# Optimization experiments

Measured on AMD Instinct MI355X. Metric: run time of the kernel, lower is better.

Reference implementation:

```python
import jax, jax.numpy as jnp
import numpy as np

B, L, C, H = 2, 2048, 1024, 16
D = C // H
THETA = 50000.0


def rotate_half(x):
    x1, x2 = jnp.split(x, 2, axis=-1)
    return jnp.concatenate((-x2, x1), axis=-1)


def rope_freqs(n, dim):
    inv_freq = 1.0 / (THETA ** (jnp.arange(0, dim, 2, dtype=jnp.float32) / dim))
    freqs = jnp.arange(n, dtype=jnp.float32)[:, None] * inv_freq[None, :]  # [n, dim//2]
    return jnp.concatenate((freqs, freqs), axis=-1)  # [n, dim]


def setup_inputs() -> dict:
    key = jax.random.key(0)
    ks = jax.random.split(key, 8)
    q = jax.random.normal(ks[0], (B, L, C), dtype=jnp.float32)
    mask = jax.random.randint(ks[1], (B, L), 0, 2) > 0
    mask = mask.at[:, 0].set(True)  # avoid fully-masked rows
    s = 1.0 / np.sqrt(C)
    Wq = jax.random.normal(ks[2], (C, C), dtype=jnp.float32) * s
    Wk = jax.random.normal(ks[3], (C, C), dtype=jnp.float32) * s
    Wv = jax.random.normal(ks[4], (C, C), dtype=jnp.float32) * s
    Wo = jax.random.normal(ks[5], (C, C), dtype=jnp.float32) * s
    bo = jnp.zeros((C,), dtype=jnp.float32)
    return {"q": q, "mask": mask, "Wq": Wq, "Wk": Wk, "Wv": Wv, "Wo": Wo, "bo": bo}


def reference(q, mask, Wq, Wk, Wv, Wo, bo):
    x = q
    # QKV projections (torch Linear: y = x @ W.T)
    def proj(W):
        y = jnp.einsum('blc,oc->blo', x, W)
        return y.reshape(B, L, H, D).transpose(0, 2, 1, 3)  # [B,H,L,D]
    qh, kh, vh = proj(Wq), proj(Wk), proj(Wv)
    # RoPE (L == S)
    pos = rope_freqs(L, D)  # [L, D]
    cos, sin = jnp.cos(pos), jnp.sin(pos)
    qh = qh * cos + rotate_half(qh) * sin
    kh = kh * cos + rotate_half(kh) * sin
    # masked SDPA with additive bias (-inf where mask is False)
    scale = 1.0 / np.sqrt(D)
    bias = jnp.where(mask[:, None, None, :], 0.0, -jnp.inf)  # [B,1,1,S]
    scores = jnp.einsum('bhld,bhsd->bhls', qh, kh) * scale + bias
    attn = jax.nn.softmax(scores, axis=-1)
    out = jnp.einsum('bhls,bhsd->bhld', attn, vh)
    out = out.transpose(0, 2, 1, 3).reshape(B, L, C)
    return jnp.einsum('blc,oc->blo', out, Wo) + bo
```

## Files before the change

kernel.cpp:

```cpp
#include <hip/hip_runtime.h>
#include <hip/hip_bf16.h>

typedef __hip_bfloat16 bf16;
typedef short bf16x8 __attribute__((ext_vector_type(8)));
typedef short bf16x4 __attribute__((ext_vector_type(4)));
typedef float floatx4 __attribute__((ext_vector_type(4)));

#define Bb 2
#define Ll 2048
#define Cc 1024
#define Hh 16
#define Dd 64
#define INVFREQ_LN 0.3381180763f
#define QSCALE 0.125f
#define NCONV 4096

#define GLD16(gp, lp) __builtin_amdgcn_global_load_lds( \
    (const __attribute__((address_space(1))) void*)(gp), \
    (__attribute__((address_space(3))) void*)(lp), 16, 0, 0)

__device__ inline short f2bf(float f) {
    __hip_bfloat16 h = __float2bfloat16(f);
    return *reinterpret_cast<short*>(&h);
}
__device__ inline short f2bf_rn(float f) {
    return (short)((__float_as_uint(f) + 0x8000u) >> 16);
}

__global__ __launch_bounds__(256) void convert_scan(
    const float* __restrict__ x, const float* __restrict__ wq,
    const float* __restrict__ wk, const float* __restrict__ wv,
    const float* __restrict__ wo,
    bf16* __restrict__ xb, bf16* __restrict__ wqkv, bf16* __restrict__ wob,
    const int* __restrict__ mask, int* __restrict__ cidx, int* __restrict__ valid)
{
    if (blockIdx.x >= NCONV) {
        const int b   = blockIdx.x - NCONV;
        const int tid = threadIdx.x;
        const int base = b * Ll + tid * 8;
        int m[8]; int s = 0;
        #pragma unroll
        for (int i = 0; i < 8; i++) { m[i] = mask[base + i] ? 1 : 0; s += m[i]; }
        const int lane = tid & 63;
        int xx = s;
        #pragma unroll
        for (int off = 1; off < 64; off <<= 1) {
            int y = __shfl_up(xx, off);
            if (lane >= off) xx += y;
        }
        __shared__ int wtot[4];
        if (lane == 63) wtot[tid >> 6] = xx;
        __syncthreads();
        int wbase = 0;
        const int w = tid >> 6;
        #pragma unroll
        for (int i = 0; i < 4; i++) if (i < w) wbase += wtot[i];
        int run = wbase + (xx - s);
        #pragma unroll
        for (int i = 0; i < 8; i++) { cidx[base + i] = run; run += m[i]; }
        if (tid == 255) valid[b] = run;
        return;
    }

    const int XN = (Bb * Ll * Cc) / 8;
    const int WN = (Cc * Cc) / 8;
    int i = blockIdx.x * 256 + threadIdx.x;
    const float* src; bf16* dst;
    if (i < XN)               { src = x  + (size_t)i * 8;                 dst = xb   + (size_t)i * 8; }
    else if (i < XN + WN)     { int j = i - XN;        src = wq + (size_t)j * 8; dst = wqkv + (size_t)j * 8; }
    else if (i < XN + 2*WN)   { int j = i - XN - WN;   src = wk + (size_t)j * 8; dst = wqkv + (size_t)Cc*Cc     + (size_t)j * 8; }
    else if (i < XN + 3*WN)   { int j = i - XN - 2*WN; src = wv + (size_t)j * 8; dst = wqkv + (size_t)Cc*Cc*2   + (size_t)j * 8; }
    else                      { int j = i - XN - 3*WN; src = wo + (size_t)j * 8; dst = wob  + (size_t)j * 8; }
    float4 a = *reinterpret_cast<const float4*>(src);
    float4 b = *reinterpret_cast<const float4*>(src + 4);
    float vv[8] = {a.x, a.y, a.z, a.w, b.x, b.y, b.z, b.w};
    bf16x8 o;
    #pragma unroll
    for (int t = 0; t < 8; t++) o[t] = f2bf(vv[t]);
    *reinterpret_cast<bf16x8*>(dst) = o;
}

template <int ROWS, int NTHREADS>
__device__ __forceinline__ void stage_swz(const bf16* __restrict__ g, int ldk,
                                          short* lds, int tid)
{
    #pragma unroll
    for (int s = 0; s < (ROWS * 4) / NTHREADS; s++) {
        const int idx = s * NTHREADS + tid;
        const int r   = idx >> 2;
        const int col = ((idx & 3) ^ ((r >> 1) & 3)) << 3;
        GLD16(g + (size_t)r * ldk + col, lds + idx * 8);
    }
}

#define SYNC_KEEP(N) do { \
    asm volatile("s_waitcnt vmcnt(" #N ")" ::: "memory"); \
    __builtin_amdgcn_s_barrier(); \
    asm volatile("" ::: "memory"); } while (0)

template <int MODE>
__global__ __launch_bounds__(256, 3) void gemm_mfma(
    const bf16* __restrict__ A, const bf16* __restrict__ W,
    bf16* __restrict__ qb, bf16* __restrict__ kb, bf16* __restrict__ vb,
    float* __restrict__ outf, const float* __restrict__ bias,
    const int* __restrict__ cmask, const int* __restrict__ cidx,
    int M, int N, int K)
{
    __shared__ __align__(16) short As[3][128 * 32];
    __shared__ __align__(16) short Bs[3][128 * 32];

    const int tid  = threadIdx.x;
    const int wave = tid >> 6;
    const int lane = tid & 63;
    const int l15  = lane & 15;
    const int quad = lane >> 4;
    const int wm   = wave >> 1;
    const int wn   = wave & 1;

    const int nbx = gridDim.x;
    const int nwg = nbx * gridDim.y;
    const int lin = blockIdx.y * nbx + blockIdx.x;
    const int cpx = nwg >> 3;
    const int swz = (lin & 7) * cpx + (lin >> 3);
    const int m0  = (swz / nbx) * 128;
    const int n0  = (swz % nbx) * 128;

    const bf16* Ag = A + (size_t)m0 * K;
    const bf16* Wg = W + (size_t)n0 * K;

    const int gsw = (quad ^ ((l15 >> 1) & 3)) << 3;

    floatx4 acc[4][4];
    #pragma unroll
    for (int mt = 0; mt < 4; mt++)
        #pragma unroll
        for (int nt = 0; nt < 4; nt++)
            #pragma unroll
            for (int r = 0; r < 4; r++) acc[mt][nt][r] = 0.f;

    const int T = K >> 5;

    stage_swz<128, 256>(Ag,      K, &As[0][0], tid);
    stage_swz<128, 256>(Wg,      K, &Bs[0][0], tid);
    stage_swz<128, 256>(Ag + 32, K, &As[1][0], tid);
    stage_swz<128, 256>(Wg + 32, K, &Bs[1][0], tid);
    SYNC_KEEP(4);

    int cur = 0;
    for (int t = 0; t < T; t++) {
        const short* Ac = &As[0][0] + cur * (128 * 32);
        const short* Bc = &Bs[0][0] + cur * (128 * 32);

        if (t + 2 < T) {
            int nb = cur + 2; if (nb >= 3) nb -= 3;
            const int kk = (t + 2) << 5;
            stage_swz<128, 256>(Ag + kk, K, &As[0][0] + nb * (128 * 32), tid);
            stage_swz<128, 256>(Wg + kk, K, &Bs[0][0] + nb * (128 * 32), tid);
        }

        bf16x8 bfr[4];
        #pragma unroll
        for (int nt = 0; nt < 4; nt++)
            bfr[nt] = *(const bf16x8*)(Bc + (wn * 64 + nt * 16 + l15) * 32 + gsw);

        __builtin_amdgcn_s_setprio(1);
        #pragma unroll
        for (int mt = 0; mt < 4; mt++) {
            bf16x8 af = *(const bf16x8*)(Ac + (wm * 64 + mt * 16 + l15) * 32 + gsw);
            #pragma unroll
            for (int nt = 0; nt < 4; nt++)
                acc[mt][nt] = __builtin_amdgcn_mfma_f32_16x16x32_bf16(
                    af, bfr[nt], acc[mt][nt], 0, 0, 0);
        }
        __builtin_amdgcn_s_setprio(0);

        if (t + 2 < T) SYNC_KEEP(4);
        else           SYNC_KEEP(0);

        cur = (cur + 1 == 3) ? 0 : cur + 1;
    }

    if constexpr (MODE == 1) {
        #pragma unroll
        for (int mt = 0; mt < 4; mt++)
            #pragma unroll
            for (int r = 0; r < 4; r++) {
                int row = m0 + wm * 64 + mt * 16 + quad * 4 + r;
                #pragma unroll
                for (int nt = 0; nt < 4; nt++) {
                    int col = n0 + wn * 64 + nt * 16 + l15;
                    outf[(size_t)row * N + col] = acc[mt][nt][r] + bias[col];
                }
            }
    } else {
        const int colbase = n0 + wn * 64;
        const int which   = colbase >> 10;
        const int hh      = (colbase & (Cc - 1)) >> 6;
        if (which == 2) {
            #pragma unroll
            for (int mt = 0; mt < 4; mt++)
                #pragma unroll
                for (int r = 0; r < 4; r++) {
                    int row = m0 + wm * 64 + mt * 16 + quad * 4 + r;
                    int b = row >> 11, l = row & (Ll - 1);
                    if (cmask[b * Ll + l]) {
                        int c = cidx[b * Ll + l];
                        size_t head = (size_t)(b * Hh + hh) * Dd * Ll;
                        int lbase = (c & ~63) | (c & 7);
                        int lg    = (c >> 3) & 7;
                        #pragma unroll
                        for (int nt = 0; nt < 4; nt++) {
                            int d = nt * 16 + l15;
                            int pos = lbase | ((lg ^ (d & 7)) << 3);
                            vb[head + (size_t)d * Ll + pos] = __float2bfloat16(acc[mt][nt][r]);
                        }
                    }
                }
        } else {
            bf16* dst = which ? kb : qb;
            const float qs = which ? 1.0f : QSCALE;
            const float base0 = __expf(-(float)l15 * INVFREQ_LN);
            const float base1 = __expf(-(float)(l15 + 16) * INVFREQ_LN);
            #pragma unroll
            for (int mt = 0; mt < 4; mt++)
                #pragma unroll
                for (int r = 0; r < 4; r++) {
                    int row = m0 + wm * 64 + mt * 16 + quad * 4 + r;
                    int b = row >> 11, l = row & (Ll - 1);
                    int cm = 1, c = l;
                    if (which == 1) {
                        cm = cmask[b * Ll + l];
                        c  = cidx[b * Ll + l];
                    }
                    if (cm) {
                        size_t rb = ((size_t)(b * Hh + hh) * Ll + c) * Dd;
                        #pragma unroll
                        for (int nt2 = 0; nt2 < 2; nt2++) {
                            float fr = (float)l * (nt2 ? base1 : base0);
                            float sn, cs;
                            __sincosf(fr, &sn, &cs);
                            float x1 = acc[mt][nt2][r];
                            float x2 = acc[mt][nt2 + 2][r];
                            float o1 = (x1 * cs - x2 * sn) * qs;
                            float o2 = (x2 * cs + x1 * sn) * qs;
                            int d1 = nt2 * 16 + l15;
                            int d2 = d1 + 32;
                            if (which == 1) {
                                int sw = c & 7;
                                int a1 = ((((d1 >> 3) ^ sw)) << 3) | (d1 & 7);
                                int a2 = ((((d2 >> 3) ^ sw)) << 3) | (d2 & 7);
                                dst[rb + a1] = __float2bfloat16(o1);
                                dst[rb + a2] = __float2bfloat16(o2);
                            } else {
                                dst[rb + d1] = __float2bfloat16(o1);
                                dst[rb + d2] = __float2bfloat16(o2);
                            }
                        }
                    }
                }
        }
    }
}

#define LSTR 72

__global__ __launch_bounds__(512) void attn_mfma(
    const bf16* __restrict__ q, const bf16* __restrict__ k, const bf16* __restrict__ vt,
    const int* __restrict__ valid, bf16* __restrict__ ctx)
{
    __shared__ __align__(16) short Ks[2][64 * 64];
    __shared__ __align__(16) short Vs[2][64 * 64];
    __shared__ __align__(16) short Ps[8][16 * LSTR];

    const int tid  = threadIdx.x;
    const int wave = tid >> 6;
    const int lane = tid & 63;
    const int l15  = lane & 15;
    const int quad = lane >> 4;

    const int bh = blockIdx.x & 31;
    const int q0 = (blockIdx.x >> 5) << 7;
    const int b  = bh >> 4;
    const int h  = bh & (Hh - 1);

    const int nvalid = valid[b];
    const int ntiles = (nvalid + 63) >> 6;

    const short* qb  = (const short*)(q  + (size_t)bh * Ll * Dd);
    const short* kb  = (const short*)(k  + (size_t)bh * Ll * Dd);
    const short* vtb = (const short*)(vt + (size_t)bh * Dd * Ll);

    const int qrow = q0 + wave * 16 + l15;
    bf16x8 qa0 = *(const bf16x8*)(qb + (size_t)qrow * Dd + quad * 8);
    bf16x8 qa1 = *(const bf16x8*)(qb + (size_t)qrow * Dd + 32 + quad * 8);

    const int g0 = ((quad ^ (l15 & 7)) << 3);
    const int g1 = (((quad + 4) ^ (l15 & 7)) << 3);

    const short* vgp = vtb + (size_t)(tid >> 3) * Ll + ((tid & 7) << 3);
    short* ksl = &Ks[0][0] + tid * 8;
    short* vsl = &Vs[0][0] + tid * 8;
    const int lbuf = 64 * 64;

    floatx4 O[4];
    float l_r = 0.f;
    #pragma unroll
    for (int nt = 0; nt < 4; nt++)
        #pragma unroll
        for (int r = 0; r < 4; r++) O[nt][r] = 0.f;

    GLD16(kb + tid * 8, ksl);
    GLD16(vgp, vsl);

    for (int t = 0; t < ntiles; t++) {
        const int cur = t & 1;
        __syncthreads();
        if (t + 1 < ntiles) {
            const int s1 = (t + 1) << 6;
            GLD16(kb + (size_t)s1 * Dd + tid * 8, ksl + (cur ^ 1) * lbuf);
            GLD16(vgp + s1,                       vsl + (cur ^ 1) * lbuf);
        }

        const short* Kc = &Ks[cur][0];
        const short* Vc = &Vs[cur][0];
        floatx4 S[4];
        #pragma unroll
        for (int nt = 0; nt < 4; nt++) {
            const short* krow = Kc + (nt * 16 + l15) * 64;
            bf16x8 ka0 = *(const bf16x8*)(krow + g0);
            bf16x8 ka1 = *(const bf16x8*)(krow + g1);
            floatx4 acc; acc[0] = acc[1] = acc[2] = acc[3] = 0.f;
            acc = __builtin_amdgcn_mfma_f32_16x16x32_bf16(ka0, qa0, acc, 0, 0, 0);
            acc = __builtin_amdgcn_mfma_f32_16x16x32_bf16(ka1, qa1, acc, 0, 0, 0);
            S[nt] = acc;
        }

        if (t + 1 < ntiles) {
            #pragma unroll
            for (int nt = 0; nt < 4; nt++) {
                bf16x4 pw;
                #pragma unroll
                for (int r = 0; r < 4; r++) {
                    float p = __expf(S[nt][r]);
                    l_r += p;
                    pw[r] = f2bf_rn(p);
                }
                *(bf16x4*)&Ps[wave][l15 * LSTR + nt * 16 + quad * 4] = pw;
            }
        } else {
            const int kbase = (t << 6) + quad * 4;
            #pragma unroll
            for (int nt = 0; nt < 4; nt++) {
                bf16x4 pw;
                #pragma unroll
                for (int r = 0; r < 4; r++) {
                    float p = (kbase + nt * 16 + r < nvalid) ? __expf(S[nt][r]) : 0.f;
                    l_r += p;
                    pw[r] = f2bf_rn(p);
                }
                *(bf16x4*)&Ps[wave][l15 * LSTR + nt * 16 + quad * 4] = pw;
            }
        }

        bf16x8 pb0 = *(const bf16x8*)&Ps[wave][l15 * LSTR + quad * 8];
        bf16x8 pb1 = *(const bf16x8*)&Ps[wave][l15 * LSTR + 32 + quad * 8];
        #pragma unroll
        for (int nt = 0; nt < 4; nt++) {
            const short* vrow = Vc + (nt * 16 + l15) * 64;
            bf16x8 va0 = *(const bf16x8*)(vrow + g0);
            bf16x8 va1 = *(const bf16x8*)(vrow + g1);
            O[nt] = __builtin_amdgcn_mfma_f32_16x16x32_bf16(va0, pb0, O[nt], 0, 0, 0);
            O[nt] = __builtin_amdgcn_mfma_f32_16x16x32_bf16(va1, pb1, O[nt], 0, 0, 0);
        }
    }

    float l = l_r;
    l += __shfl_xor(l, 16);
    l += __shfl_xor(l, 32);
    const float inv = 1.0f / l;

    {
        int row = q0 + wave * 16 + l15;
        short* cp = (short*)ctx + ((size_t)(b * Ll + row)) * Cc + h * Dd;
        #pragma unroll
        for (int nt = 0; nt < 4; nt++) {
            bf16x4 ov;
            #pragma unroll
            for (int r = 0; r < 4; r++) ov[r] = f2bf_rn(O[nt][r] * inv);
            *(bf16x4*)&cp[nt * 16 + quad * 4] = ov;
        }
    }
}

extern "C" void kernel_launch(void* const* d_in, const int* in_sizes, int n_in,
                              void* d_out, int out_size, void* d_ws, size_t ws_size,
                              hipStream_t stream) {
    const float* x    = (const float*)d_in[0];
    const int*   mask = (const int*)d_in[1];
    const float* Wq   = (const float*)d_in[2];
    const float* Wk   = (const float*)d_in[3];
    const float* Wv   = (const float*)d_in[4];
    const float* Wo   = (const float*)d_in[5];
    const float* bo   = (const float*)d_in[6];
    float* out = (float*)d_out;

    const size_t per = (size_t)Bb * Hh * Ll * Dd;
    bf16* qbuf = (bf16*)d_ws;
    bf16* kbuf = qbuf + per;
    bf16* vbuf = kbuf + per;
    bf16* xb   = vbuf + per;
    bf16* wqkv = xb + per;
    bf16* wob  = wqkv + (size_t)3 * Cc * Cc;
    int*  cidx   = (int*)(wob + (size_t)Cc * Cc);
    int*  cvalid = cidx + Bb * Ll;
    bf16* ctx  = xb;

    const int M = Bb * Ll;

    convert_scan<<<NCONV + Bb, 256, 0, stream>>>(
        x, Wq, Wk, Wv, Wo, xb, wqkv, wob, mask, cidx, cvalid);

    dim3 gQKV(3 * Cc / 128, M / 128);
    gemm_mfma<0><<<gQKV, 256, 0, stream>>>(xb, wqkv, qbuf, kbuf, vbuf,
                                           nullptr, nullptr, mask, cidx, M, 3 * Cc, Cc);

    attn_mfma<<<Bb * Hh * (Ll / 128), 512, 0, stream>>>(qbuf, kbuf, vbuf, cvalid, ctx);

    dim3 gOut(Cc / 128, M / 128);
    gemm_mfma<1><<<gOut, 256, 0, stream>>>(ctx, wob, nullptr, nullptr, nullptr,
                                           out, bo, nullptr, nullptr, M, Cc, Cc);
}
```

Baseline: 178.2 us.

## Split GEMM into specialized QKV 256x256 tile and output 64x128 tile kernels

Replaces the templated 128x128 GEMM with two specialized kernels. The QKV projection now uses 512-thread blocks with 256x256 tiles and a ping-pong schedule, splitting each k-step into two MFMA halves separated by barriers and interleaved with staged loads. The output projection uses smaller 64x128 tiles so it launches more blocks and fills the GPU better. The changes aim to raise data reuse and MFMA utilization in the large GEMM and occupancy in the small one, at the cost of more LDS, more registers and extra barriers per iteration.

```diff
diff --git a/kernel.cpp b/kernel.cpp
--- a/kernel.cpp
+++ b/kernel.cpp
@@ -93,20 +93,175 @@
     }
 }
 
-#define SYNC_KEEP(N) do { \
-    asm volatile("s_waitcnt vmcnt(" #N ")" ::: "memory"); \
-    __builtin_amdgcn_s_barrier(); \
-    asm volatile("" ::: "memory"); } while (0)
-
-template <int MODE>
-__global__ __launch_bounds__(256, 3) void gemm_mfma(
+#define VMCNT(N) asm volatile("s_waitcnt vmcnt(" #N ")" ::: "memory")
+
+__global__ __launch_bounds__(512, 2) void gemm_qkv(
     const bf16* __restrict__ A, const bf16* __restrict__ W,
     bf16* __restrict__ qb, bf16* __restrict__ kb, bf16* __restrict__ vb,
-    float* __restrict__ outf, const float* __restrict__ bias,
-    const int* __restrict__ cmask, const int* __restrict__ cidx,
-    int M, int N, int K)
+    const int* __restrict__ cmask, const int* __restrict__ cidx)
 {
-    __shared__ __align__(16) short As[3][128 * 32];
+    constexpr int K = Cc;
+    constexpr int T = K / 32;
+
+    __shared__ __align__(16) short As[3][256 * 32];
+    __shared__ __align__(16) short Bs[3][256 * 32];
+
+    const int tid  = threadIdx.x;
+    const int wave = tid >> 6;
+    const int lane = tid & 63;
+    const int l15  = lane & 15;
+    const int quad = lane >> 4;
+    const int wm   = wave >> 2;
+    const int wn   = wave & 3;
+
+    const int lin = blockIdx.y * 12 + blockIdx.x;
+    const int swz = (lin & 7) * 24 + (lin >> 3);
+    const int m0  = (swz / 12) * 256;
+    const int n0  = (swz % 12) * 256;
+
+    const bf16* Ag = A + (size_t)m0 * K;
+    const bf16* Wg = W + (size_t)n0 * K;
+
+    const int gsw = (quad ^ ((l15 >> 1) & 3)) << 3;
+
+    floatx4 acc[8][4];
+    #pragma unroll
+    for (int mt = 0; mt < 8; mt++)
+        #pragma unroll
+        for (int nt = 0; nt < 4; nt++)
+            #pragma unroll
+            for (int r = 0; r < 4; r++) acc[mt][nt][r] = 0.f;
+
+    stage_swz<256, 512>(Ag,      K, &As[0][0], tid);
+    stage_swz<256, 512>(Wg,      K, &Bs[0][0], tid);
+    stage_swz<256, 512>(Ag + 32, K, &As[1][0], tid);
+    stage_swz<256, 512>(Wg + 32, K, &Bs[1][0], tid);
+    VMCNT(4);
+    __builtin_amdgcn_s_barrier();
+
+    int cur = 0;
+    for (int t = 0; t < T; t++) {
+        const short* Ac = &As[0][0] + cur * (256 * 32);
+        const short* Bc = &Bs[0][0] + cur * (256 * 32);
+        int nb = cur + 2; if (nb >= 3) nb -= 3;
+        const int kk = (t + 2) << 5;
+
+        bf16x8 bfr[4], af[4];
+        #pragma unroll
+        for (int nt = 0; nt < 4; nt++)
+            bfr[nt] = *(const bf16x8*)(Bc + (wn * 64 + nt * 16 + l15) * 32 + gsw);
+        #pragma unroll
+        for (int mt = 0; mt < 4; mt++)
+            af[mt] = *(const bf16x8*)(Ac + (wm * 128 + mt * 16 + l15) * 32 + gsw);
+        if (t + 2 < T) stage_swz<256, 512>(Ag + kk, K, &As[nb][0], tid);
+        __builtin_amdgcn_s_barrier();
+        __builtin_amdgcn_s_setprio(1);
+        #pragma unroll
+        for (int mt = 0; mt < 4; mt++)
+            #pragma unroll
+            for (int nt = 0; nt < 4; nt++)
+                acc[mt][nt] = __builtin_amdgcn_mfma_f32_16x16x32_bf16(
+                    af[mt], bfr[nt], acc[mt][nt], 0, 0, 0);
+        __builtin_amdgcn_s_setprio(0);
+        __builtin_amdgcn_s_barrier();
+
+        bf16x8 ag[4];
+        #pragma unroll
+        for (int mt = 0; mt < 4; mt++)
+            ag[mt] = *(const bf16x8*)(Ac + (wm * 128 + (mt + 4) * 16 + l15) * 32 + gsw);
+        if (t + 2 < T) stage_swz<256, 512>(Wg + kk, K, &Bs[nb][0], tid);
+        __builtin_amdgcn_s_barrier();
+        __builtin_amdgcn_s_setprio(1);
+        #pragma unroll
+        for (int mt = 0; mt < 4; mt++)
+            #pragma unroll
+            for (int nt = 0; nt < 4; nt++)
+                acc[mt + 4][nt] = __builtin_amdgcn_mfma_f32_16x16x32_bf16(
+                    ag[mt], bfr[nt], acc[mt + 4][nt], 0, 0, 0);
+        __builtin_amdgcn_s_setprio(0);
+        if (t + 2 < T) { VMCNT(4); }
+        else           { VMCNT(0); }
+        __builtin_amdgcn_s_barrier();
+
+        cur++; if (cur == 3) cur = 0;
+    }
+
+    const int colbase = n0 + wn * 64;
+    const int which   = colbase >> 10;
+    const int hh      = (colbase & (Cc - 1)) >> 6;
+    if (which == 2) {
+        #pragma unroll
+        for (int mt = 0; mt < 8; mt++)
+            #pragma unroll
+            for (int r = 0; r < 4; r++) {
+                int row = m0 + wm * 128 + mt * 16 + quad * 4 + r;
+                int b = row >> 11, l = row & (Ll - 1);
+                if (cmask[b * Ll + l]) {
+                    int c = cidx[b * Ll + l];
+                    size_t head = (size_t)(b * Hh + hh) * Dd * Ll;
+                    int lbase = (c & ~63) | (c & 7);
+                    int lg    = (c >> 3) & 7;
+                    #pragma unroll
+                    for (int nt = 0; nt < 4; nt++) {
+                        int d = nt * 16 + l15;
+                        int pos = lbase | ((lg ^ (d & 7)) << 3);
+                        vb[head + (size_t)d * Ll + pos] = __float2bfloat16(acc[mt][nt][r]);
+                    }
+                }
+            }
+    } else {
+        bf16* dst = which ? kb : qb;
+        const float qs = which ? 1.0f : QSCALE;
+        const float base0 = __expf(-(float)l15 * INVFREQ_LN);
+        const float base1 = __expf(-(float)(l15 + 16) * INVFREQ_LN);
+        #pragma unroll
+        for (int mt = 0; mt < 8; mt++)
+            #pragma unroll
+            for (int r = 0; r < 4; r++) {
+                int row = m0 + wm * 128 + mt * 16 + quad * 4 + r;
+                int b = row >> 11, l = row & (Ll - 1);
+                int cm = 1, c = l;
+                if (which == 1) {
+                    cm = cmask[b * Ll + l];
+                    c  = cidx[b * Ll + l];
+                }
+                if (cm) {
+                    size_t rb = ((size_t)(b * Hh + hh) * Ll + c) * Dd;
+                    #pragma unroll
+                    for (int nt2 = 0; nt2 < 2; nt2++) {
+                        float fr = (float)l * (nt2 ? base1 : base0);
+                        float sn, cs;
+                        __sincosf(fr, &sn, &cs);
+                        float x1 = acc[mt][nt2][r];
+                        float x2 = acc[mt][nt2 + 2][r];
+                        float o1 = (x1 * cs - x2 * sn) * qs;
+                        float o2 = (x2 * cs + x1 * sn) * qs;
+                        int d1 = nt2 * 16 + l15;
+                        int d2 = d1 + 32;
+                        if (which == 1) {
+                            int sw = c & 7;
+                            int a1 = ((((d1 >> 3) ^ sw)) << 3) | (d1 & 7);
+                            int a2 = ((((d2 >> 3) ^ sw)) << 3) | (d2 & 7);
+                            dst[rb + a1] = __float2bfloat16(o1);
+                            dst[rb + a2] = __float2bfloat16(o2);
+                        } else {
+                            dst[rb + d1] = __float2bfloat16(o1);
+                            dst[rb + d2] = __float2bfloat16(o2);
+                        }
+                    }
+                }
+            }
+    }
+}
+
+__global__ __launch_bounds__(256, 2) void gemm_out(
+    const bf16* __restrict__ A, const bf16* __restrict__ W,
+    float* __restrict__ outf, const float* __restrict__ bias)
+{
+    constexpr int K = Cc, N = Cc;
+    constexpr int T = K / 32;
+
+    __shared__ __align__(16) short As[3][64 * 32];
     __shared__ __align__(16) short Bs[3][128 * 32];
 
     const int tid  = threadIdx.x;
@@ -117,149 +272,78 @@
     const int wm   = wave >> 1;
     const int wn   = wave & 1;
 
-    const int nbx = gridDim.x;
-    const int nwg = nbx * gridDim.y;
-    const int lin = blockIdx.y * nbx + blockIdx.x;
-    const int cpx = nwg >> 3;
-    const int swz = (lin & 7) * cpx + (lin >> 3);
-    const int m0  = (swz / nbx) * 128;
-    const int n0  = (swz % nbx) * 128;
+    const int lin = blockIdx.y * 8 + blockIdx.x;
+    const int swz = (lin & 7) * 64 + (lin >> 3);
+    const int m0  = (swz >> 3) * 64;
+    const int n0  = (swz & 7) * 128;
 
     const bf16* Ag = A + (size_t)m0 * K;
     const bf16* Wg = W + (size_t)n0 * K;
 
     const int gsw = (quad ^ ((l15 >> 1) & 3)) << 3;
 
-    floatx4 acc[4][4];
+    floatx4 acc[2][4];
     #pragma unroll
-    for (int mt = 0; mt < 4; mt++)
+    for (int mt = 0; mt < 2; mt++)
         #pragma unroll
         for (int nt = 0; nt < 4; nt++)
             #pragma unroll
             for (int r = 0; r < 4; r++) acc[mt][nt][r] = 0.f;
 
-    const int T = K >> 5;
-
-    stage_swz<128, 256>(Ag,      K, &As[0][0], tid);
+    stage_swz<64,  256>(Ag,      K, &As[0][0], tid);
     stage_swz<128, 256>(Wg,      K, &Bs[0][0], tid);
-    stage_swz<128, 256>(Ag + 32, K, &As[1][0], tid);
+    stage_swz<64,  256>(Ag + 32, K, &As[1][0], tid);
     stage_swz<128, 256>(Wg + 32, K, &Bs[1][0], tid);
-    SYNC_KEEP(4);
+    VMCNT(3);
+    __builtin_amdgcn_s_barrier();
 
     int cur = 0;
     for (int t = 0; t < T; t++) {
-        const short* Ac = &As[0][0] + cur * (128 * 32);
+        const short* Ac = &As[0][0] + cur * (64 * 32);
         const short* Bc = &Bs[0][0] + cur * (128 * 32);
 
         if (t + 2 < T) {
             int nb = cur + 2; if (nb >= 3) nb -= 3;
             const int kk = (t + 2) << 5;
-            stage_swz<128, 256>(Ag + kk, K, &As[0][0] + nb * (128 * 32), tid);
-            stage_swz<128, 256>(Wg + kk, K, &Bs[0][0] + nb * (128 * 32), tid);
-        }
-
-        bf16x8 bfr[4];
+            stage_swz<64,  256>(Ag + kk, K, &As[nb][0], tid);
+            stage_swz<128, 256>(Wg + kk, K, &Bs[nb][0], tid);
+        }
+
+        bf16x8 af[2], bfr[4];
+        #pragma unroll
+        for (int mt = 0; mt < 2; mt++)
+            af[mt] = *(const bf16x8*)(Ac + (wm * 32 + mt * 16 + l15) * 32 + gsw);
         #pragma unroll
         for (int nt = 0; nt < 4; nt++)
             bfr[nt] = *(const bf16x8*)(Bc + (wn * 64 + nt * 16 + l15) * 32 + gsw);
 
         __builtin_amdgcn_s_setprio(1);
         #pragma unroll
-        for (int mt = 0; mt < 4; mt++) {
-            bf16x8 af = *(const bf16x8*)(Ac + (wm * 64 + mt * 16 + l15) * 32 + gsw);
+        for (int mt = 0; mt < 2; mt++)
             #pragma unroll
             for (int nt = 0; nt < 4; nt++)
                 acc[mt][nt] = __builtin_amdgcn_mfma_f32_16x16x32_bf16(
-                    af, bfr[nt], acc[mt][nt], 0, 0, 0);
-        }
+                    af[mt], bfr[nt], acc[mt][nt], 0, 0, 0);
         __builtin_amdgcn_s_setprio(0);
 
-        if (t + 2 < T) SYNC_KEEP(4);
-        else           SYNC_KEEP(0);
-
-        cur = (cur + 1 == 3) ? 0 : cur + 1;
-    }
-
-    if constexpr (MODE == 1) {
-        #pragma unroll
-        for (int mt = 0; mt < 4; mt++)
-            #pragma unroll
-            for (int r = 0; r < 4; r++) {
-                int row = m0 + wm * 64 + mt * 16 + quad * 4 + r;
-                #pragma unroll
-                for (int nt = 0; nt < 4; nt++) {
-                    int col = n0 + wn * 64 + nt * 16 + l15;
-                    outf[(size_t)row * N + col] = acc[mt][nt][r] + bias[col];
-                }
+        if (t + 2 < T) { VMCNT(3); }
+        else           { VMCNT(0); }
+        __builtin_amdgcn_s_barrier();
+
+        cur++; if (cur == 3) cur = 0;
+    }
+
+    #pragma unroll
+    for (int mt = 0; mt < 2; mt++)
+        #pragma unroll
+        for (int r = 0; r < 4; r++) {
+            int row = m0 + wm * 32 + mt * 16 + quad * 4 + r;
+            #pragma unroll
+            for (int nt = 0; nt < 4; nt++) {
+                int col = n0 + wn * 64 + nt * 16 + l15;
+                outf[(size_t)row * N + col] = acc[mt][nt][r] + bias[col];
             }
-    } else {
-        const int colbase = n0 + wn * 64;
-        const int which   = colbase >> 10;
-        const int hh      = (colbase & (Cc - 1)) >> 6;
-        if (which == 2) {
-            #pragma unroll
-            for (int mt = 0; mt < 4; mt++)
-                #pragma unroll
-                for (int r = 0; r < 4; r++) {
-                    int row = m0 + wm * 64 + mt * 16 + quad * 4 + r;
-                    int b = row >> 11, l = row & (Ll - 1);
-                    if (cmask[b * Ll + l]) {
-                        int c = cidx[b * Ll + l];
-                        size_t head = (size_t)(b * Hh + hh) * Dd * Ll;
-                        int lbase = (c & ~63) | (c & 7);
-                        int lg    = (c >> 3) & 7;
-                        #pragma unroll
-                        for (int nt = 0; nt < 4; nt++) {
-                            int d = nt * 16 + l15;
-                            int pos = lbase | ((lg ^ (d & 7)) << 3);
-                            vb[head + (size_t)d * Ll + pos] = __float2bfloat16(acc[mt][nt][r]);
-                        }
-                    }
-                }
-        } else {
-            bf16* dst = which ? kb : qb;
-            const float qs = which ? 1.0f : QSCALE;
-            const float base0 = __expf(-(float)l15 * INVFREQ_LN);
-            const float base1 = __expf(-(float)(l15 + 16) * INVFREQ_LN);
-            #pragma unroll
-            for (int mt = 0; mt < 4; mt++)
-                #pragma unroll
-                for (int r = 0; r < 4; r++) {
-                    int row = m0 + wm * 64 + mt * 16 + quad * 4 + r;
-                    int b = row >> 11, l = row & (Ll - 1);
-                    int cm = 1, c = l;
-                    if (which == 1) {
-                        cm = cmask[b * Ll + l];
-                        c  = cidx[b * Ll + l];
-                    }
-                    if (cm) {
-                        size_t rb = ((size_t)(b * Hh + hh) * Ll + c) * Dd;
-                        #pragma unroll
-                        for (int nt2 = 0; nt2 < 2; nt2++) {
-                            float fr = (float)l * (nt2 ? base1 : base0);
-                            float sn, cs;
-                            __sincosf(fr, &sn, &cs);
-                            float x1 = acc[mt][nt2][r];
-                            float x2 = acc[mt][nt2 + 2][r];
-                            float o1 = (x1 * cs - x2 * sn) * qs;
-                            float o2 = (x2 * cs + x1 * sn) * qs;
-                            int d1 = nt2 * 16 + l15;
-                            int d2 = d1 + 32;
-                            if (which == 1) {
-                                int sw = c & 7;
-                                int a1 = ((((d1 >> 3) ^ sw)) << 3) | (d1 & 7);
-                                int a2 = ((((d2 >> 3) ^ sw)) << 3) | (d2 & 7);
-                                dst[rb + a1] = __float2bfloat16(o1);
-                                dst[rb + a2] = __float2bfloat16(o2);
-                            } else {
-                                dst[rb + d1] = __float2bfloat16(o1);
-                                dst[rb + d2] = __float2bfloat16(o2);
-                            }
-                        }
-                    }
-                }
-        }
-    }
+        }
 }
 
 #define LSTR 72
@@ -420,13 +504,11 @@
     convert_scan<<<NCONV + Bb, 256, 0, stream>>>(
         x, Wq, Wk, Wv, Wo, xb, wqkv, wob, mask, cidx, cvalid);
 
-    dim3 gQKV(3 * Cc / 128, M / 128);
-    gemm_mfma<0><<<gQKV, 256, 0, stream>>>(xb, wqkv, qbuf, kbuf, vbuf,
-                                           nullptr, nullptr, mask, cidx, M, 3 * Cc, Cc);
+    dim3 gQKV(3 * Cc / 256, M / 256);
+    gemm_qkv<<<gQKV, 512, 0, stream>>>(xb, wqkv, qbuf, kbuf, vbuf, mask, cidx);
 
     attn_mfma<<<Bb * Hh * (Ll / 128), 512, 0, stream>>>(qbuf, kbuf, vbuf, cvalid, ctx);
 
-    dim3 gOut(Cc / 128, M / 128);
-    gemm_mfma<1><<<gOut, 256, 0, stream>>>(ctx, wob, nullptr, nullptr, nullptr,
-                                           out, bo, nullptr, nullptr, M, Cc, Cc);
-}
+    dim3 gOut(Cc / 128, M / 64);
+    gemm_out<<<gOut, 256, 0, stream>>>(ctx, wob, out, bo);
+}
```

After: 184.2 us. +3.4%, slower.

## Split-K output GEMM with atomics and deepen QKV GEMM K-tile to 64

Applied to the files above, without the earlier changes.

The QKV projection moves to a dedicated kernel with 64-wide K tiles, double-buffered LDS and a new XOR swizzle, which halves the barrier count per K step. The output projection is split along K into two halves that accumulate into the fp32 output with atomic adds, doubling the number of workgroups from 256. The output buffer is zeroed by extra blocks in the convert kernel. In exchange, the atomics add memory traffic and make the sum order nondeterministic, and the larger LDS tiles lower occupancy.

```diff
diff --git a/kernel.cpp b/kernel.cpp
--- a/kernel.cpp
+++ b/kernel.cpp
@@ -14,6 +14,7 @@
 #define INVFREQ_LN 0.3381180763f
 #define QSCALE 0.125f
 #define NCONV 4096
+#define NZERO 2048
 
 #define GLD16(gp, lp) __builtin_amdgcn_global_load_lds( \
     (const __attribute__((address_space(1))) void*)(gp), \
@@ -32,10 +33,11 @@
     const float* __restrict__ wk, const float* __restrict__ wv,
     const float* __restrict__ wo,
     bf16* __restrict__ xb, bf16* __restrict__ wqkv, bf16* __restrict__ wob,
+    float* __restrict__ outz,
     const int* __restrict__ mask, int* __restrict__ cidx, int* __restrict__ valid)
 {
-    if (blockIdx.x >= NCONV) {
-        const int b   = blockIdx.x - NCONV;
+    if (blockIdx.x >= NCONV + NZERO) {
+        const int b   = blockIdx.x - NCONV - NZERO;
         const int tid = threadIdx.x;
         const int base = b * Ll + tid * 8;
         int m[8]; int s = 0;
@@ -59,6 +61,13 @@
         #pragma unroll
         for (int i = 0; i < 8; i++) { cidx[base + i] = run; run += m[i]; }
         if (tid == 255) valid[b] = run;
+        return;
+    }
+    if (blockIdx.x >= NCONV) {
+        const int i = (blockIdx.x - NCONV) * 2048 + threadIdx.x * 8;
+        float4 z; z.x = z.y = z.z = z.w = 0.f;
+        *reinterpret_cast<float4*>(outz + i) = z;
+        *reinterpret_cast<float4*>(outz + i + 4) = z;
         return;
     }
 
@@ -93,21 +102,31 @@
     }
 }
 
-#define SYNC_KEEP(N) do { \
-    asm volatile("s_waitcnt vmcnt(" #N ")" ::: "memory"); \
-    __builtin_amdgcn_s_barrier(); \
-    asm volatile("" ::: "memory"); } while (0)
-
-template <int MODE>
-__global__ __launch_bounds__(256, 3) void gemm_mfma(
+template <int NTHREADS>
+__device__ __forceinline__ void stage64_swz(const bf16* __restrict__ g, int ldk,
+                                            short* lds, int tid)
+{
+    #pragma unroll
+    for (int s = 0; s < (128 * 8) / NTHREADS; s++) {
+        const int idx = s * NTHREADS + tid;
+        const int r   = idx >> 3;
+        const int col = ((idx & 7) ^ (r & 7)) << 3;
+        GLD16(g + (size_t)r * ldk + col, lds + idx * 8);
+    }
+}
+
+#define VMCNT(N) asm volatile("s_waitcnt vmcnt(" #N ")" ::: "memory")
+
+__global__ __launch_bounds__(256, 2) void gemm_qkv(
     const bf16* __restrict__ A, const bf16* __restrict__ W,
     bf16* __restrict__ qb, bf16* __restrict__ kb, bf16* __restrict__ vb,
-    float* __restrict__ outf, const float* __restrict__ bias,
-    const int* __restrict__ cmask, const int* __restrict__ cidx,
-    int M, int N, int K)
+    const int* __restrict__ cmask, const int* __restrict__ cidx)
 {
-    __shared__ __align__(16) short As[3][128 * 32];
-    __shared__ __align__(16) short Bs[3][128 * 32];
+    constexpr int K = Cc;
+    constexpr int T = K / 64;
+
+    __shared__ __align__(16) short As[2][128 * 64];
+    __shared__ __align__(16) short Bs[2][128 * 64];
 
     const int tid  = threadIdx.x;
     const int wave = tid >> 6;
@@ -117,17 +136,155 @@
     const int wm   = wave >> 1;
     const int wn   = wave & 1;
 
-    const int nbx = gridDim.x;
-    const int nwg = nbx * gridDim.y;
-    const int lin = blockIdx.y * nbx + blockIdx.x;
-    const int cpx = nwg >> 3;
-    const int swz = (lin & 7) * cpx + (lin >> 3);
-    const int m0  = (swz / nbx) * 128;
-    const int n0  = (swz % nbx) * 128;
+    const int lin = blockIdx.y * 24 + blockIdx.x;
+    const int swz = (lin & 7) * 96 + (lin >> 3);
+    const int m0  = (swz / 24) * 128;
+    const int n0  = (swz % 24) * 128;
 
     const bf16* Ag = A + (size_t)m0 * K;
     const bf16* Wg = W + (size_t)n0 * K;
 
+    floatx4 acc[4][4];
+    #pragma unroll
+    for (int mt = 0; mt < 4; mt++)
+        #pragma unroll
+        for (int nt = 0; nt < 4; nt++)
+            #pragma unroll
+            for (int r = 0; r < 4; r++) acc[mt][nt][r] = 0.f;
+
+    stage64_swz<256>(Ag, K, &As[0][0], tid);
+    stage64_swz<256>(Wg, K, &Bs[0][0], tid);
+
+    for (int t = 0; t < T; t++) {
+        const int cur = t & 1;
+        __builtin_amdgcn_s_barrier();
+        if (t + 1 < T) {
+            stage64_swz<256>(Ag + (t + 1) * 64, K, &As[cur ^ 1][0], tid);
+            stage64_swz<256>(Wg + (t + 1) * 64, K, &Bs[cur ^ 1][0], tid);
+            VMCNT(8);
+        } else {
+            VMCNT(0);
+        }
+
+        const short* Ac = &As[cur][0];
+        const short* Bc = &Bs[cur][0];
+        #pragma unroll
+        for (int kk = 0; kk < 2; kk++) {
+            const int gsw = ((kk * 4 + quad) ^ (l15 & 7)) << 3;
+            bf16x8 af[4], bfv[4];
+            #pragma unroll
+            for (int mt = 0; mt < 4; mt++)
+                af[mt] = *(const bf16x8*)(Ac + (wm * 64 + mt * 16 + l15) * 64 + gsw);
+            #pragma unroll
+            for (int nt = 0; nt < 4; nt++)
+                bfv[nt] = *(const bf16x8*)(Bc + (wn * 64 + nt * 16 + l15) * 64 + gsw);
+            __builtin_amdgcn_s_setprio(1);
+            #pragma unroll
+            for (int mt = 0; mt < 4; mt++)
+                #pragma unroll
+                for (int nt = 0; nt < 4; nt++)
+                    acc[mt][nt] = __builtin_amdgcn_mfma_f32_16x16x32_bf16(
+                        af[mt], bfv[nt], acc[mt][nt], 0, 0, 0);
+            __builtin_amdgcn_s_setprio(0);
+        }
+    }
+
+    const int colbase = n0 + wn * 64;
+    const int which   = colbase >> 10;
+    const int hh      = (colbase & (Cc - 1)) >> 6;
+    if (which == 2) {
+        #pragma unroll
+        for (int mt = 0; mt < 4; mt++)
+            #pragma unroll
+            for (int r = 0; r < 4; r++) {
+                int row = m0 + wm * 64 + mt * 16 + quad * 4 + r;
+                int b = row >> 11, l = row & (Ll - 1);
+                if (cmask[b * Ll + l]) {
+                    int c = cidx[b * Ll + l];
+                    size_t head = (size_t)(b * Hh + hh) * Dd * Ll;
+                    int lbase = (c & ~63) | (c & 7);
+                    int lg    = (c >> 3) & 7;
+                    #pragma unroll
+                    for (int nt = 0; nt < 4; nt++) {
+                        int d = nt * 16 + l15;
+                        int pos = lbase | ((lg ^ (d & 7)) << 3);
+                        vb[head + (size_t)d * Ll + pos] = __float2bfloat16(acc[mt][nt][r]);
+                    }
+                }
+            }
+    } else {
+        bf16* dst = which ? kb : qb;
+        const float qs = which ? 1.0f : QSCALE;
+        const float base0 = __expf(-(float)l15 * INVFREQ_LN);
+        const float base1 = __expf(-(float)(l15 + 16) * INVFREQ_LN);
+        #pragma unroll
+        for (int mt = 0; mt < 4; mt++)
+            #pragma unroll
+            for (int r = 0; r < 4; r++) {
+                int row = m0 + wm * 64 + mt * 16 + quad * 4 + r;
+                int b = row >> 11, l = row & (Ll - 1);
+                int cm = 1, c = l;
+                if (which == 1) {
+                    cm = cmask[b * Ll + l];
+                    c  = cidx[b * Ll + l];
+                }
+                if (cm) {
+                    size_t rb = ((size_t)(b * Hh + hh) * Ll + c) * Dd;
+                    #pragma unroll
+                    for (int nt2 = 0; nt2 < 2; nt2++) {
+                        float fr = (float)l * (nt2 ? base1 : base0);
+                        float sn, cs;
+                        __sincosf(fr, &sn, &cs);
+                        float x1 = acc[mt][nt2][r];
+                        float x2 = acc[mt][nt2 + 2][r];
+                        float o1 = (x1 * cs - x2 * sn) * qs;
+                        float o2 = (x2 * cs + x1 * sn) * qs;
+                        int d1 = nt2 * 16 + l15;
+                        int d2 = d1 + 32;
+                        if (which == 1) {
+                            int sw = c & 7;
+                            int a1 = ((((d1 >> 3) ^ sw)) << 3) | (d1 & 7);
+                            int a2 = ((((d2 >> 3) ^ sw)) << 3) | (d2 & 7);
+                            dst[rb + a1] = __float2bfloat16(o1);
+                            dst[rb + a2] = __float2bfloat16(o2);
+                        } else {
+                            dst[rb + d1] = __float2bfloat16(o1);
+                            dst[rb + d2] = __float2bfloat16(o2);
+                        }
+                    }
+                }
+            }
+    }
+}
+
+__global__ __launch_bounds__(256, 2) void gemm_out(
+    const bf16* __restrict__ A, const bf16* __restrict__ W,
+    float* __restrict__ outf, const float* __restrict__ bias)
+{
+    constexpr int N = Cc;
+    constexpr int KS = Cc / 2;
+    constexpr int T  = KS / 32;
+
+    __shared__ __align__(16) short As[3][128 * 32];
+    __shared__ __align__(16) short Bs[3][128 * 32];
+
+    const int tid  = threadIdx.x;
+    const int wave = tid >> 6;
+    const int lane = tid & 63;
+    const int l15  = lane & 15;
+    const int quad = lane >> 4;
+    const int wm   = wave >> 1;
+    const int wn   = wave & 1;
+    const int ks   = blockIdx.z;
+
+    const int lin = blockIdx.y * 8 + blockIdx.x;
+    const int swz = (lin & 7) * 32 + (lin >> 3);
+    const int m0  = (swz >> 3) * 128;
+    const int n0  = (swz & 7) * 128;
+
+    const bf16* Ag = A + (size_t)m0 * Cc + ks * KS;
+    const bf16* Wg = W + (size_t)n0 * Cc + ks * KS;
+
     const int gsw = (quad ^ ((l15 >> 1) & 3)) << 3;
 
     floatx4 acc[4][4];
@@ -138,13 +295,12 @@
             #pragma unroll
             for (int r = 0; r < 4; r++) acc[mt][nt][r] = 0.f;
 
-    const int T = K >> 5;
-
-    stage_swz<128, 256>(Ag,      K, &As[0][0], tid);
-    stage_swz<128, 256>(Wg,      K, &Bs[0][0], tid);
-    stage_swz<128, 256>(Ag + 32, K, &As[1][0], tid);
-    stage_swz<128, 256>(Wg + 32, K, &Bs[1][0], tid);
-    SYNC_KEEP(4);
+    stage_swz<128, 256>(Ag,      Cc, &As[0][0], tid);
+    stage_swz<128, 256>(Wg,      Cc, &Bs[0][0], tid);
+    stage_swz<128, 256>(Ag + 32, Cc, &As[1][0], tid);
+    stage_swz<128, 256>(Wg + 32, Cc, &Bs[1][0], tid);
+    VMCNT(4);
+    __builtin_amdgcn_s_barrier();
 
     int cur = 0;
     for (int t = 0; t < T; t++) {
@@ -154,112 +310,46 @@
         if (t + 2 < T) {
             int nb = cur + 2; if (nb >= 3) nb -= 3;
             const int kk = (t + 2) << 5;
-            stage_swz<128, 256>(Ag + kk, K, &As[0][0] + nb * (128 * 32), tid);
-            stage_swz<128, 256>(Wg + kk, K, &Bs[0][0] + nb * (128 * 32), tid);
-        }
-
-        bf16x8 bfr[4];
+            stage_swz<128, 256>(Ag + kk, Cc, &As[nb][0], tid);
+            stage_swz<128, 256>(Wg + kk, Cc, &Bs[nb][0], tid);
+        }
+
+        bf16x8 af[4], bfr[4];
+        #pragma unroll
+        for (int mt = 0; mt < 4; mt++)
+            af[mt] = *(const bf16x8*)(Ac + (wm * 64 + mt * 16 + l15) * 32 + gsw);
         #pragma unroll
         for (int nt = 0; nt < 4; nt++)
             bfr[nt] = *(const bf16x8*)(Bc + (wn * 64 + nt * 16 + l15) * 32 + gsw);
 
         __builtin_amdgcn_s_setprio(1);
         #pragma unroll
-        for (int mt = 0; mt < 4; mt++) {
-            bf16x8 af = *(const bf16x8*)(Ac + (wm * 64 + mt * 16 + l15) * 32 + gsw);
+        for (int mt = 0; mt < 4; mt++)
             #pragma unroll
             for (int nt = 0; nt < 4; nt++)
                 acc[mt][nt] = __builtin_amdgcn_mfma_f32_16x16x32_bf16(
-                    af, bfr[nt], acc[mt][nt], 0, 0, 0);
-        }
+                    af[mt], bfr[nt], acc[mt][nt], 0, 0, 0);
         __builtin_amdgcn_s_setprio(0);
 
-        if (t + 2 < T) SYNC_KEEP(4);
-        else           SYNC_KEEP(0);
-
-        cur = (cur + 1 == 3) ? 0 : cur + 1;
-    }
-
-    if constexpr (MODE == 1) {
-        #pragma unroll
-        for (int mt = 0; mt < 4; mt++)
-            #pragma unroll
-            for (int r = 0; r < 4; r++) {
-                int row = m0 + wm * 64 + mt * 16 + quad * 4 + r;
-                #pragma unroll
-                for (int nt = 0; nt < 4; nt++) {
-                    int col = n0 + wn * 64 + nt * 16 + l15;
-                    outf[(size_t)row * N + col] = acc[mt][nt][r] + bias[col];
-                }
+        if (t + 2 < T) { VMCNT(4); }
+        else           { VMCNT(0); }
+        __builtin_amdgcn_s_barrier();
+
+        cur++; if (cur == 3) cur = 0;
+    }
+
+    #pragma unroll
+    for (int mt = 0; mt < 4; mt++)
+        #pragma unroll
+        for (int r = 0; r < 4; r++) {
+            int row = m0 + wm * 64 + mt * 16 + quad * 4 + r;
+            #pragma unroll
+            for (int nt = 0; nt < 4; nt++) {
+                int col = n0 + wn * 64 + nt * 16 + l15;
+                float v = acc[mt][nt][r] + (ks == 0 ? bias[col] : 0.f);
+                unsafeAtomicAdd(&outf[(size_t)row * N + col], v);
             }
-    } else {
-        const int colbase = n0 + wn * 64;
-        const int which   = colbase >> 10;
-        const int hh      = (colbase & (Cc - 1)) >> 6;
-        if (which == 2) {
-            #pragma unroll
-            for (int mt = 0; mt < 4; mt++)
-                #pragma unroll
-                for (int r = 0; r < 4; r++) {
-                    int row = m0 + wm * 64 + mt * 16 + quad * 4 + r;
-                    int b = row >> 11, l = row & (Ll - 1);
-                    if (cmask[b * Ll + l]) {
-                        int c = cidx[b * Ll + l];
-                        size_t head = (size_t)(b * Hh + hh) * Dd * Ll;
-                        int lbase = (c & ~63) | (c & 7);
-                        int lg    = (c >> 3) & 7;
-                        #pragma unroll
-                        for (int nt = 0; nt < 4; nt++) {
-                            int d = nt * 16 + l15;
-                            int pos = lbase | ((lg ^ (d & 7)) << 3);
-                            vb[head + (size_t)d * Ll + pos] = __float2bfloat16(acc[mt][nt][r]);
-                        }
-                    }
-                }
-        } else {
-            bf16* dst = which ? kb : qb;
-            const float qs = which ? 1.0f : QSCALE;
-            const float base0 = __expf(-(float)l15 * INVFREQ_LN);
-            const float base1 = __expf(-(float)(l15 + 16) * INVFREQ_LN);
-            #pragma unroll
-            for (int mt = 0; mt < 4; mt++)
-                #pragma unroll
-                for (int r = 0; r < 4; r++) {
-                    int row = m0 + wm * 64 + mt * 16 + quad * 4 + r;
-                    int b = row >> 11, l = row & (Ll - 1);
-                    int cm = 1, c = l;
-                    if (which == 1) {
-                        cm = cmask[b * Ll + l];
-                        c  = cidx[b * Ll + l];
-                    }
-                    if (cm) {
-                        size_t rb = ((size_t)(b * Hh + hh) * Ll + c) * Dd;
-                        #pragma unroll
-                        for (int nt2 = 0; nt2 < 2; nt2++) {
-                            float fr = (float)l * (nt2 ? base1 : base0);
-                            float sn, cs;
-                            __sincosf(fr, &sn, &cs);
-                            float x1 = acc[mt][nt2][r];
-                            float x2 = acc[mt][nt2 + 2][r];
-                            float o1 = (x1 * cs - x2 * sn) * qs;
-                            float o2 = (x2 * cs + x1 * sn) * qs;
-                            int d1 = nt2 * 16 + l15;
-                            int d2 = d1 + 32;
-                            if (which == 1) {
-                                int sw = c & 7;
-                                int a1 = ((((d1 >> 3) ^ sw)) << 3) | (d1 & 7);
-                                int a2 = ((((d2 >> 3) ^ sw)) << 3) | (d2 & 7);
-                                dst[rb + a1] = __float2bfloat16(o1);
-                                dst[rb + a2] = __float2bfloat16(o2);
-                            } else {
-                                dst[rb + d1] = __float2bfloat16(o1);
-                                dst[rb + d2] = __float2bfloat16(o2);
-                            }
-                        }
-                    }
-                }
-        }
-    }
+        }
 }
 
 #define LSTR 72
@@ -417,16 +507,14 @@
 
     const int M = Bb * Ll;
 
-    convert_scan<<<NCONV + Bb, 256, 0, stream>>>(
-        x, Wq, Wk, Wv, Wo, xb, wqkv, wob, mask, cidx, cvalid);
+    convert_scan<<<NCONV + NZERO + Bb, 256, 0, stream>>>(
+        x, Wq, Wk, Wv, Wo, xb, wqkv, wob, out, mask, cidx, cvalid);
 
     dim3 gQKV(3 * Cc / 128, M / 128);
-    gemm_mfma<0><<<gQKV, 256, 0, stream>>>(xb, wqkv, qbuf, kbuf, vbuf,
-                                           nullptr, nullptr, mask, cidx, M, 3 * Cc, Cc);
+    gemm_qkv<<<gQKV, 256, 0, stream>>>(xb, wqkv, qbuf, kbuf, vbuf, mask, cidx);
 
     attn_mfma<<<Bb * Hh * (Ll / 128), 512, 0, stream>>>(qbuf, kbuf, vbuf, cvalid, ctx);
 
-    dim3 gOut(Cc / 128, M / 128);
-    gemm_mfma<1><<<gOut, 256, 0, stream>>>(ctx, wob, nullptr, nullptr, nullptr,
-                                           out, bo, nullptr, nullptr, M, Cc, Cc);
-}
+    dim3 gOut(Cc / 128, M / 128, 2);
+    gemm_out<<<gOut, 256, 0, stream>>>(ctx, wob, out, bo);
+}
```

Result: slower. 206.1 us (+15.7%).
